# Performance work log

Measured on AMD Instinct MI355X. Metric: run time of the kernel, lower is better.

Reference implementation:

```python
import jax, jax.numpy as jnp
import numpy as np

V, T, E, H, B, S = 50000, 45, 256, 512, 32, 256


def setup_inputs() -> dict:
    key = jax.random.key(0)
    ks = jax.random.split(key, 14)
    s = 0.05
    return dict(
        x=jax.random.randint(ks[0], (B, S), 0, V),
        tags=jax.random.randint(ks[1], (B, S), 0, T),
        mask=jnp.ones((B, S), dtype=bool),
        emb=jax.random.normal(ks[2], (V, E), jnp.float32),
        Wih_f=jax.random.normal(ks[3], (4 * H, E), jnp.float32) * s,
        Whh_f=jax.random.normal(ks[4], (4 * H, H), jnp.float32) * s,
        bih_f=jnp.zeros((4 * H,), jnp.float32),
        bhh_f=jnp.zeros((4 * H,), jnp.float32),
        Wih_b=jax.random.normal(ks[5], (4 * H, E), jnp.float32) * s,
        Whh_b=jax.random.normal(ks[6], (4 * H, H), jnp.float32) * s,
        bih_b=jnp.zeros((4 * H,), jnp.float32),
        bhh_b=jnp.zeros((4 * H,), jnp.float32),
        Wout=jax.random.normal(ks[7], (T, 2 * H), jnp.float32) * s,
        bout=jnp.zeros((T,), jnp.float32),
        start=jax.random.normal(ks[8], (T,), jnp.float32) * 0.1,
        end=jax.random.normal(ks[9], (T,), jnp.float32) * 0.1,
        trans=jax.random.normal(ks[10], (T, T), jnp.float32) * 0.1,
    )


def _lstm_dir(xp, Whh, reverse):
    # xp: [S, B, 4H] precomputed input projection + biases; gate order i,f,g,o (torch)
    Bn = xp.shape[1]
    Hn = Whh.shape[1]
    def step(carry, g_in):
        h, c = carry
        g = g_in + h @ Whh.T
        i, f, gg, o = jnp.split(g, 4, axis=-1)
        c = jax.nn.sigmoid(f) * c + jax.nn.sigmoid(i) * jnp.tanh(gg)
        h = jax.nn.sigmoid(o) * jnp.tanh(c)
        return (h, c), h
    init = (jnp.zeros((Bn, Hn), xp.dtype), jnp.zeros((Bn, Hn), xp.dtype))
    _, hs = jax.lax.scan(step, init, xp, reverse=reverse)
    return hs  # [S, B, H]


def _crf_nll(emissions, tags, mask, start, end, trans):
    # emissions: [B, S, T]; neg mean log-likelihood (torchcrf, reduction='mean')
    mf = mask.astype(emissions.dtype)
    em_tag = jnp.take_along_axis(emissions, tags[:, :, None], axis=2)[:, :, 0]  # [B,S]
    num = start[tags[:, 0]] + em_tag[:, 0]
    num = num + ((trans[tags[:, :-1], tags[:, 1:]] + em_tag[:, 1:]) * mf[:, 1:]).sum(1)
    seq_ends = mf.sum(1).astype(tags.dtype) - 1
    last_tags = jnp.take_along_axis(tags, seq_ends[:, None], axis=1)[:, 0]
    num = num + end[last_tags]
    def denom_step(alpha, inp):
        em_t, m_t = inp  # [B,T], [B]
        nxt = jax.nn.logsumexp(alpha[:, :, None] + trans[None, :, :] + em_t[:, None, :], axis=1)
        return jnp.where(m_t[:, None] > 0, nxt, alpha), None
    alpha0 = start[None, :] + emissions[:, 0]
    em_rest = emissions.transpose(1, 0, 2)[1:]  # [S-1, B, T]
    alpha, _ = jax.lax.scan(denom_step, alpha0, (em_rest, mf.T[1:]))
    logZ = jax.nn.logsumexp(alpha + end[None, :], axis=1)
    return -(num - logZ).mean()


def reference(x, tags, mask, emb, Wih_f, Whh_f, bih_f, bhh_f,
              Wih_b, Whh_b, bih_b, bhh_b, Wout, bout, start, end, trans):
    embeds = emb[x]                      # [B, S, E]
    xs = embeds.transpose(1, 0, 2)       # [S, B, E]
    xp_f = jnp.einsum('sbe,ge->sbg', xs, Wih_f) + bih_f + bhh_f
    hs_f = _lstm_dir(xp_f, Whh_f, False)
    xp_b = jnp.einsum('sbe,ge->sbg', xs, Wih_b) + bih_b + bhh_b
    hs_b = _lstm_dir(xp_b, Whh_b, True)
    hcat = jnp.concatenate([hs_f, hs_b], axis=-1)          # [S, B, 2H]
    emissions = jnp.einsum('sbh,th->sbt', hcat, Wout) + bout
    emissions = emissions.transpose(1, 0, 2)                # [B, S, T]
    return _crf_nll(emissions, tags, mask, start, end, trans)
```

## Files before the change

### kernel.cpp

```cpp
#include <hip/hip_runtime.h>
#include <stdint.h>

#define S_LEN 256
#define B_N 32
#define H_N 512
#define E_N 256
#define T_N 45
#define G4H 2048

typedef unsigned short u16;
typedef u16 u16x8 __attribute__((ext_vector_type(8)));
typedef u16 u16x4 __attribute__((ext_vector_type(4)));
typedef __bf16 bf16x8 __attribute__((ext_vector_type(8)));
typedef float f32x4 __attribute__((ext_vector_type(4)));
typedef unsigned long long u64;

#define OFF_BAR   0ull
#define OFF_ATOK  256ull
#define OFF_WIHF  (OFF_ATOK + 4194304ull)
#define OFF_WIHB  (OFF_WIHF + 1048576ull)
#define OFF_WHHF  (OFF_WIHB + 1048576ull)
#define OFF_WHHB  (OFF_WHHF + 2097152ull)
#define OFF_WOUT  (OFF_WHHB + 2097152ull)
#define OFF_BSF   (OFF_WOUT + 98304ull)
#define OFF_BSB   (OFF_BSF + 8192ull)
#define OFF_XPF   (OFF_BSB + 8192ull)
#define OFF_XPB   (OFF_XPF + 33554432ull)
#define OFF_HSF   (OFF_XPB + 33554432ull)
#define OFF_HSB   (OFF_HSF + 8421376ull)
#define OFF_EM    (OFF_HSB + 8421376ull)
#define OFF_VAL   (OFF_EM + 1572864ull)

__device__ __forceinline__ u16 f2bf(float f) {
  union { float f; unsigned u; } v; v.f = f;
  unsigned r = v.u + 0x7FFFu + ((v.u >> 16) & 1u);
  return (u16)(r >> 16);
}
__device__ __forceinline__ float bf2f(u16 b) {
  union { unsigned u; float f; } v; v.u = ((unsigned)b) << 16;
  return v.f;
}
__device__ __forceinline__ bf16x8 ld8(const u16* p) {
  u16x8 v = *reinterpret_cast<const u16x8*>(p);
  return __builtin_bit_cast(bf16x8, v);
}
__device__ __forceinline__ void st_h8(u16* p, u16x4 v) {
  __hip_atomic_store(reinterpret_cast<u64*>(p), __builtin_bit_cast(u64, v),
                     __ATOMIC_RELAXED, __HIP_MEMORY_SCOPE_AGENT);
}
__device__ __forceinline__ bf16x8 ld_h16(const u16* p) {
  u64 lo = __hip_atomic_load(reinterpret_cast<const u64*>(p),
                             __ATOMIC_RELAXED, __HIP_MEMORY_SCOPE_AGENT);
  u64 hi = __hip_atomic_load(reinterpret_cast<const u64*>(p + 4),
                             __ATOMIC_RELAXED, __HIP_MEMORY_SCOPE_AGENT);
  union { u64 q[2]; u16x8 v; } u;
  u.q[0] = lo; u.q[1] = hi;
  return __builtin_bit_cast(bf16x8, u.v);
}
__device__ __forceinline__ f32x4 mfma16(bf16x8 a, bf16x8 b, f32x4 c) {
  return __builtin_amdgcn_mfma_f32_16x16x32_bf16(a, b, c, 0, 0, 0);
}
__device__ __forceinline__ float sigm(float x) { return 1.f / (1.f + __expf(-x)); }
__device__ __forceinline__ float tanhf_(float x) {
  float ax = fabsf(x);
  float e = __expf(-2.f * ax);
  float t = 1.f - 2.f * e / (1.f + e);
  return (x < 0.f) ? -t : t;
}
__device__ __forceinline__ float wredmax(float v) {
  #pragma unroll
  for (int m = 1; m < 64; m <<= 1) v = fmaxf(v, __shfl_xor(v, m));
  return v;
}
__device__ __forceinline__ float wredsum(float v) {
  #pragma unroll
  for (int m = 1; m < 64; m <<= 1) v += __shfl_xor(v, m);
  return v;
}

__global__ void k_castA(const int* __restrict__ x, const float* __restrict__ emb,
                        u16* __restrict__ atok) {
  int idx = blockIdx.x * 256 + threadIdx.x;
  int t = idx >> 5;
  int e0 = (idx & 31) << 3;
  int s = t >> 5, b = t & 31;
  int xid = x[b * S_LEN + s];
  const float4* p = reinterpret_cast<const float4*>(emb + (size_t)xid * E_N + e0);
  float4 lo = p[0], hi = p[1];
  u16x8 o;
  o[0] = f2bf(lo.x); o[1] = f2bf(lo.y); o[2] = f2bf(lo.z); o[3] = f2bf(lo.w);
  o[4] = f2bf(hi.x); o[5] = f2bf(hi.y); o[6] = f2bf(hi.z); o[7] = f2bf(hi.w);
  *reinterpret_cast<u16x8*>(atok + (size_t)t * E_N + e0) = o;
}

__global__ void k_castW(const float* __restrict__ WihF, const float* __restrict__ WihB,
                        const float* __restrict__ WhhF, const float* __restrict__ WhhB,
                        const float* __restrict__ Wout,
                        const float* __restrict__ bihF, const float* __restrict__ bhhF,
                        const float* __restrict__ bihB, const float* __restrict__ bhhB,
                        u16* wihf, u16* wihb, u16* whhf, u16* whhb, u16* woutp,
                        float* bsf, float* bsb, u16* hsf, u16* hsb) {
  int i = blockIdx.x * 256 + threadIdx.x;
  if (i < 524288) { wihf[i] = f2bf(WihF[i]); return; }
  i -= 524288;
  if (i < 524288) { wihb[i] = f2bf(WihB[i]); return; }
  i -= 524288;
  if (i < 1048576) { whhf[i] = f2bf(WhhF[i]); return; }
  i -= 1048576;
  if (i < 1048576) { whhb[i] = f2bf(WhhB[i]); return; }
  i -= 1048576;
  if (i < 49152) {
    int n = i >> 10, k = i & 1023;
    woutp[i] = (n < T_N) ? f2bf(Wout[n * 1024 + k]) : (u16)0;
    return;
  }
  i -= 49152;
  if (i < 2048) { bsf[i] = bihF[i] + bhhF[i]; return; }
  i -= 2048;
  if (i < 2048) { bsb[i] = bihB[i] + bhhB[i]; return; }
  i -= 2048;
  if (i < 16384) { hsf[i] = 0; return; }
  i -= 16384;
  if (i < 16384) { hsb[(size_t)256 * 16384 + i] = 0; return; }
}

__global__ __launch_bounds__(256) void k_gemm_xp(
    const u16* __restrict__ atok, const u16* __restrict__ wihF, const u16* __restrict__ wihB,
    const float* __restrict__ bsF, const float* __restrict__ bsB,
    u16* __restrict__ xpF, u16* __restrict__ xpB) {
  int wid = blockIdx.x;
  int dir = wid >> 10, rem = wid & 1023;
  const int wave = threadIdx.x >> 6, lane = threadIdx.x & 63;
  const int lr = lane & 15, lh = lane >> 4;
  const int t0 = (rem >> 3) * 64;
  const int g0 = (rem & 7) * 256 + wave * 64;
  const u16* wih = dir ? wihB : wihF;
  const float* bs = dir ? bsB : bsF;
  u16* xp = dir ? xpB : xpF;
  f32x4 acc[4][4] = {};
  for (int kk = 0; kk < 8; ++kk) {
    int e = kk * 32 + lh * 8;
    bf16x8 a[4], bfr[4];
    #pragma unroll
    for (int mi = 0; mi < 4; ++mi) a[mi] = ld8(atok + (size_t)(t0 + 16 * mi + lr) * E_N + e);
    #pragma unroll
    for (int ni = 0; ni < 4; ++ni) bfr[ni] = ld8(wih + (size_t)(g0 + 16 * ni + lr) * E_N + e);
    #pragma unroll
    for (int mi = 0; mi < 4; ++mi)
      #pragma unroll
      for (int ni = 0; ni < 4; ++ni) acc[mi][ni] = mfma16(a[mi], bfr[ni], acc[mi][ni]);
  }
  #pragma unroll
  for (int ni = 0; ni < 4; ++ni) {
    int g = g0 + 16 * ni + lr;
    float bsv = bs[g];
    #pragma unroll
    for (int mi = 0; mi < 4; ++mi)
      #pragma unroll
      for (int r = 0; r < 4; ++r) {
        int t = t0 + 16 * mi + 4 * lh + r;
        xp[(size_t)t * G4H + g] = f2bf(acc[mi][ni][r] + bsv);
      }
  }
}

__global__ __launch_bounds__(128, 1) void k_lstm(
    const u16* __restrict__ whhF, const u16* __restrict__ whhB,
    const u16* __restrict__ xpF, const u16* __restrict__ xpB,
    u16* __restrict__ hsF, u16* __restrict__ hsB, int* bar) {
  const int dir = blockIdx.x >> 5;
  const int w = blockIdx.x & 31;
  const int nt = threadIdx.x >> 6;
  const int lane = threadIdx.x & 63;
  const int lr = lane & 15, lh = lane >> 4;
  const u16* whh = dir ? whhB : whhF;
  const u16* xp = dir ? xpB : xpF;
  u16* hs = dir ? hsB : hsF;
  int* cnt = bar + dir * 32;

  bf16x8 A[4][16];
  #pragma unroll
  for (int mt = 0; mt < 4; ++mt) {
    const u16* base = whh + (size_t)(mt * 512 + 16 * w + lr) * H_N + lh * 8;
    #pragma unroll
    for (int kk = 0; kk < 16; ++kk) A[mt][kk] = ld8(base + kk * 32);
  }
  const int b = nt * 16 + lr;
  const int j0 = 16 * w + 4 * lh;
  float cst[4] = {0.f, 0.f, 0.f, 0.f};

  for (int t = 0; t < S_LEN; ++t) {
    const int s = dir ? (S_LEN - 1 - t) : t;
    const int slot_r = dir ? (s + 1) : s;
    const int slot_w = dir ? s : (s + 1);
    u16x4 xq[4];
    const u16* xpt = xp + ((size_t)(s * B_N + b)) * G4H + j0;
    #pragma unroll
    for (int mt = 0; mt < 4; ++mt) xq[mt] = *reinterpret_cast<const u16x4*>(xpt + mt * 512);
    if (t > 0) {
      const int target = 32 * t;
      while (__hip_atomic_load(cnt, __ATOMIC_RELAXED, __HIP_MEMORY_SCOPE_AGENT) < target)
        __builtin_amdgcn_s_sleep(1);
    }
    const u16* hp = hs + ((size_t)slot_r * B_N + b) * H_N + lh * 8;
    bf16x8 Bf[16];
    #pragma unroll
    for (int kk = 0; kk < 16; ++kk) Bf[kk] = ld_h16(hp + kk * 32);
    f32x4 acc[4] = {};
    #pragma unroll
    for (int kk = 0; kk < 16; ++kk) {
      #pragma unroll
      for (int mt = 0; mt < 4; ++mt) acc[mt] = mfma16(A[mt][kk], Bf[kk], acc[mt]);
    }
    u16x4 hv;
    #pragma unroll
    for (int r = 0; r < 4; ++r) {
      float gi = acc[0][r] + bf2f(xq[0][r]);
      float gf = acc[1][r] + bf2f(xq[1][r]);
      float gg = acc[2][r] + bf2f(xq[2][r]);
      float go = acc[3][r] + bf2f(xq[3][r]);
      float c = sigm(gf) * cst[r] + sigm(gi) * tanhf_(gg);
      cst[r] = c;
      hv[r] = f2bf(sigm(go) * tanhf_(c));
    }
    st_h8(hs + ((size_t)slot_w * B_N + b) * H_N + j0, hv);
    __syncthreads();
    if (threadIdx.x == 0)
      __hip_atomic_fetch_add(cnt, 1, __ATOMIC_RELAXED, __HIP_MEMORY_SCOPE_AGENT);
  }
}

__global__ __launch_bounds__(256) void k_gemm_em(
    const u16* __restrict__ hsF, const u16* __restrict__ hsB,
    const u16* __restrict__ woutp, const float* __restrict__ bout, float* __restrict__ em) {
  const int wave = threadIdx.x >> 6, lane = threadIdx.x & 63;
  const int lr = lane & 15, lh = lane >> 4;
  const int t0 = blockIdx.x * 64 + wave * 16;
  f32x4 acc[3] = {};
  for (int kk = 0; kk < 32; ++kk) {
    int k = kk * 32 + lh * 8;
    int t = t0 + lr;
    int s = t >> 5, bt = t & 31;
    const u16* ap = (kk < 16) ? (hsF + ((size_t)(s + 1) * B_N + bt) * H_N + k)
                              : (hsB + ((size_t)s * B_N + bt) * H_N + (k - 512));
    bf16x8 a = ld8(ap);
    #pragma unroll
    for (int ni = 0; ni < 3; ++ni) {
      bf16x8 bb = ld8(woutp + (size_t)(16 * ni + lr) * 1024 + k);
      acc[ni] = mfma16(a, bb, acc[ni]);
    }
  }
  #pragma unroll
  for (int ni = 0; ni < 3; ++ni) {
    int tag = 16 * ni + lr;
    float bo = (tag < T_N) ? bout[tag] : 0.f;
    #pragma unroll
    for (int r = 0; r < 4; ++r) {
      int t = t0 + 4 * lh + r;
      em[(size_t)t * 48 + tag] = acc[ni][r] + bo;
    }
  }
}

__global__ __launch_bounds__(256) void k_crf(
    const float* __restrict__ em, const int* __restrict__ tags,
    const float* __restrict__ start, const float* __restrict__ endv,
    const float* __restrict__ trans, float* __restrict__ val) {
  __shared__ float tl[T_N * T_N];
  __shared__ float al[64];
  __shared__ float part[4][64];
  const int b = blockIdx.x;
  const int tid = threadIdx.x, wq = tid >> 6, lane = tid & 63;
  for (int i = tid; i < T_N * T_N; i += 256) tl[i] = trans[i];
  __syncthreads();
  float acur = (lane < T_N) ? (start[lane] + em[(size_t)b * 48 + lane]) : -1e30f;
  float shift = wredmax(acur);
  if (wq == 0) al[lane] = acur;
  __syncthreads();
  const int tbeg = wq * 12;
  const int tend = (tbeg + 12 < T_N) ? (tbeg + 12) : T_N;
  for (int s = 1; s < S_LEN; ++s) {
    float sm = 0.f;
    if (lane < T_N) {
      for (int t = tbeg; t < tend; ++t)
        sm += __expf(al[t] + tl[t * T_N + lane] - shift);
    }
    part[wq][lane] = sm;
    __syncthreads();
    float tot = part[0][lane] + part[1][lane] + part[2][lane] + part[3][lane];
    float anew = -1e30f;
    if (lane < T_N) anew = shift + __logf(tot) + em[((size_t)s * B_N + b) * 48 + lane];
    acur = anew;
    shift = wredmax(acur);
    __syncthreads();
    if (wq == 0) al[lane] = acur;
    __syncthreads();
  }
  float z = (lane < T_N) ? (acur + endv[lane]) : -1e30f;
  float m = wredmax(z);
  float sum = wredsum((lane < T_N) ? __expf(z - m) : 0.f);
  float logZ = m + __logf(sum);
  if (wq == 0) {
    float np = 0.f;
    #pragma unroll
    for (int q = 0; q < 4; ++q) {
      int s = 1 + lane * 4 + q;
      if (s < S_LEN) {
        int tp = tags[b * S_LEN + s - 1], tc = tags[b * S_LEN + s];
        np += tl[tp * T_N + tc] + em[((size_t)s * B_N + b) * 48 + tc];
      }
    }
    np = wredsum(np);
    if (lane == 0) {
      int tg0 = tags[b * S_LEN], tgL = tags[b * S_LEN + S_LEN - 1];
      float num = start[tg0] + em[(size_t)b * 48 + tg0] + np + endv[tgL];
      val[b] = num - logZ;
    }
  }
}

__global__ void k_final(const float* __restrict__ val, float* __restrict__ out) {
  int lane = threadIdx.x & 63;
  float v = (lane < B_N) ? val[lane] : 0.f;
  v = wredsum(v);
  if (threadIdx.x == 0) out[0] = -(v / (float)B_N);
}

extern "C" void kernel_launch(void* const* d_in, const int* in_sizes, int n_in,
                              void* d_out, int out_size, void* d_ws, size_t ws_size,
                              hipStream_t stream) {
  const int* x = (const int*)d_in[0];
  const int* tags = (const int*)d_in[1];
  const float* emb = (const float*)d_in[3];
  const float* WihF = (const float*)d_in[4];
  const float* WhhF = (const float*)d_in[5];
  const float* bihF = (const float*)d_in[6];
  const float* bhhF = (const float*)d_in[7];
  const float* WihB = (const float*)d_in[8];
  const float* WhhB = (const float*)d_in[9];
  const float* bihB = (const float*)d_in[10];
  const float* bhhB = (const float*)d_in[11];
  const float* Wout = (const float*)d_in[12];
  const float* bout = (const float*)d_in[13];
  const float* start = (const float*)d_in[14];
  const float* endv = (const float*)d_in[15];
  const float* trans = (const float*)d_in[16];
  float* out = (float*)d_out;
  char* ws = (char*)d_ws;

  u16* atok = (u16*)(ws + OFF_ATOK);
  u16* wihf = (u16*)(ws + OFF_WIHF);
  u16* wihb = (u16*)(ws + OFF_WIHB);
  u16* whhf = (u16*)(ws + OFF_WHHF);
  u16* whhb = (u16*)(ws + OFF_WHHB);
  u16* woutp = (u16*)(ws + OFF_WOUT);
  float* bsf = (float*)(ws + OFF_BSF);
  float* bsb = (float*)(ws + OFF_BSB);
  u16* xpf = (u16*)(ws + OFF_XPF);
  u16* xpb = (u16*)(ws + OFF_XPB);
  u16* hsf = (u16*)(ws + OFF_HSF);
  u16* hsb = (u16*)(ws + OFF_HSB);
  float* emis = (float*)(ws + OFF_EM);
  float* val = (float*)(ws + OFF_VAL);

  hipMemsetAsync(ws + OFF_BAR, 0, 256, stream);
  k_castA<<<1024, 256, 0, stream>>>(x, emb, atok);
  k_castW<<<12624, 256, 0, stream>>>(WihF, WihB, WhhF, WhhB, Wout, bihF, bhhF, bihB, bhhB,
                                     wihf, wihb, whhf, whhb, woutp, bsf, bsb, hsf, hsb);
  k_gemm_xp<<<2048, 256, 0, stream>>>(atok, wihf, wihb, bsf, bsb, xpf, xpb);
  k_lstm<<<64, 128, 0, stream>>>(whhf, whhb, xpf, xpb, hsf, hsb, (int*)(ws + OFF_BAR));
  k_gemm_em<<<128, 256, 0, stream>>>(hsf, hsb, woutp, bout, emis);
  k_crf<<<32, 256, 0, stream>>>(emis, tags, start, endv, trans, val);
  k_final<<<1, 64, 0, stream>>>(val, out);
}
```

Measured before the change: 1.528 ms.

## Replace LSTM step counter barrier with sentinel-polled hidden-state flags

Drops the per-step atomic counter barrier between the 32 LSTM blocks. The hidden-state buffers are now pre-filled with a 0xFF sentinel, and each wave spins on cache-bypassing loads of the previous h slice until no sentinel words remain. This removes the __syncthreads, the atomic increment and the separate flag poll, so data arrival itself acts as the signal. The cost is two 8 MB memsets and repeated full 256-byte reloads while spinning. Correctness relies on real bf16 pairs never equalling 0xFFFFFFFF (a NaN pattern) and on each 8-byte store becoming visible atomically.

New measurement: 1.618 ms. 5.9% more time.

```diff
diff --git a/kernel.cpp b/kernel.cpp
--- a/kernel.cpp
+++ b/kernel.cpp
@@ -9,13 +9,14 @@
 #define G4H 2048
 
 typedef unsigned short u16;
+typedef unsigned int u32;
 typedef u16 u16x8 __attribute__((ext_vector_type(8)));
 typedef u16 u16x4 __attribute__((ext_vector_type(4)));
+typedef u32 u32x4 __attribute__((ext_vector_type(4)));
 typedef __bf16 bf16x8 __attribute__((ext_vector_type(8)));
 typedef float f32x4 __attribute__((ext_vector_type(4)));
 typedef unsigned long long u64;
 
-#define OFF_BAR   0ull
 #define OFF_ATOK  256ull
 #define OFF_WIHF  (OFF_ATOK + 4194304ull)
 #define OFF_WIHB  (OFF_WIHF + 1048576ull)
@@ -48,14 +49,11 @@
   __hip_atomic_store(reinterpret_cast<u64*>(p), __builtin_bit_cast(u64, v),
                      __ATOMIC_RELAXED, __HIP_MEMORY_SCOPE_AGENT);
 }
-__device__ __forceinline__ bf16x8 ld_h16(const u16* p) {
-  u64 lo = __hip_atomic_load(reinterpret_cast<const u64*>(p),
-                             __ATOMIC_RELAXED, __HIP_MEMORY_SCOPE_AGENT);
-  u64 hi = __hip_atomic_load(reinterpret_cast<const u64*>(p + 4),
-                             __ATOMIC_RELAXED, __HIP_MEMORY_SCOPE_AGENT);
-  union { u64 q[2]; u16x8 v; } u;
-  u.q[0] = lo; u.q[1] = hi;
-  return __builtin_bit_cast(bf16x8, u.v);
+__device__ __forceinline__ u32x4 ld16cc(const u16* p) {
+  u32x4 r;
+  asm volatile("global_load_dwordx4 %0, %1, off sc0 sc1"
+               : "=v"(r) : "v"(p) : "memory");
+  return r;
 }
 __device__ __forceinline__ f32x4 mfma16(bf16x8 a, bf16x8 b, f32x4 c) {
   return __builtin_amdgcn_mfma_f32_16x16x32_bf16(a, b, c, 0, 0, 0);
@@ -167,7 +165,7 @@
 __global__ __launch_bounds__(128, 1) void k_lstm(
     const u16* __restrict__ whhF, const u16* __restrict__ whhB,
     const u16* __restrict__ xpF, const u16* __restrict__ xpB,
-    u16* __restrict__ hsF, u16* __restrict__ hsB, int* bar) {
+    u16* __restrict__ hsF, u16* __restrict__ hsB) {
   const int dir = blockIdx.x >> 5;
   const int w = blockIdx.x & 31;
   const int nt = threadIdx.x >> 6;
@@ -176,7 +174,6 @@
   const u16* whh = dir ? whhB : whhF;
   const u16* xp = dir ? xpB : xpF;
   u16* hs = dir ? hsB : hsF;
-  int* cnt = bar + dir * 32;
 
   bf16x8 A[4][16];
   #pragma unroll
@@ -197,20 +194,29 @@
     const u16* xpt = xp + ((size_t)(s * B_N + b)) * G4H + j0;
     #pragma unroll
     for (int mt = 0; mt < 4; ++mt) xq[mt] = *reinterpret_cast<const u16x4*>(xpt + mt * 512);
-    if (t > 0) {
-      const int target = 32 * t;
-      while (__hip_atomic_load(cnt, __ATOMIC_RELAXED, __HIP_MEMORY_SCOPE_AGENT) < target)
-        __builtin_amdgcn_s_sleep(1);
-    }
+
     const u16* hp = hs + ((size_t)slot_r * B_N + b) * H_N + lh * 8;
-    bf16x8 Bf[16];
-    #pragma unroll
-    for (int kk = 0; kk < 16; ++kk) Bf[kk] = ld_h16(hp + kk * 32);
+    u32x4 raw[16];
+    while (true) {
+      #pragma unroll
+      for (int kk = 0; kk < 16; ++kk) raw[kk] = ld16cc(hp + kk * 32);
+      asm volatile("s_waitcnt vmcnt(0)" ::: "memory");
+      __builtin_amdgcn_sched_barrier(0);
+      u32 bad = 0;
+      #pragma unroll
+      for (int kk = 0; kk < 16; ++kk) {
+        #pragma unroll
+        for (int d = 0; d < 4; ++d) bad |= (raw[kk][d] == 0xFFFFFFFFu) ? 1u : 0u;
+      }
+      if (__all(bad == 0)) break;
+    }
+
     f32x4 acc[4] = {};
     #pragma unroll
     for (int kk = 0; kk < 16; ++kk) {
-      #pragma unroll
-      for (int mt = 0; mt < 4; ++mt) acc[mt] = mfma16(A[mt][kk], Bf[kk], acc[mt]);
+      bf16x8 Bf = __builtin_bit_cast(bf16x8, raw[kk]);
+      #pragma unroll
+      for (int mt = 0; mt < 4; ++mt) acc[mt] = mfma16(A[mt][kk], Bf, acc[mt]);
     }
     u16x4 hv;
     #pragma unroll
@@ -224,9 +230,6 @@
       hv[r] = f2bf(sigm(go) * tanhf_(c));
     }
     st_h8(hs + ((size_t)slot_w * B_N + b) * H_N + j0, hv);
-    __syncthreads();
-    if (threadIdx.x == 0)
-      __hip_atomic_fetch_add(cnt, 1, __ATOMIC_RELAXED, __HIP_MEMORY_SCOPE_AGENT);
   }
 }
 
@@ -363,12 +366,13 @@
   float* emis = (float*)(ws + OFF_EM);
   float* val = (float*)(ws + OFF_VAL);
 
-  hipMemsetAsync(ws + OFF_BAR, 0, 256, stream);
+  hipMemsetAsync(ws + OFF_HSF + 32768ull, 0xFF, 8388608ull, stream);
+  hipMemsetAsync(ws + OFF_HSB, 0xFF, 8388608ull, stream);
   k_castA<<<1024, 256, 0, stream>>>(x, emb, atok);
   k_castW<<<12624, 256, 0, stream>>>(WihF, WihB, WhhF, WhhB, Wout, bihF, bhhF, bihB, bhhB,
                                      wihf, wihb, whhf, whhb, woutp, bsf, bsb, hsf, hsb);
   k_gemm_xp<<<2048, 256, 0, stream>>>(atok, wihf, wihb, bsf, bsb, xpf, xpb);
-  k_lstm<<<64, 128, 0, stream>>>(whhf, whhb, xpf, xpb, hsf, hsb, (int*)(ws + OFF_BAR));
+  k_lstm<<<64, 128, 0, stream>>>(whhf, whhb, xpf, xpb, hsf, hsb);
   k_gemm_em<<<128, 256, 0, stream>>>(hsf, hsb, woutp, bout, emis);
   k_crf<<<32, 256, 0, stream>>>(emis, tags, start, endv, trans, val);
   k_final<<<1, 64, 0, stream>>>(val, out);
```
